# Optimization experiments

Measured on AMD Instinct MI355X. Metric: run time of the kernel, lower is better.

The kernel has to match this reference:

```python
import jax, jax.numpy as jnp
import numpy as np

N = 20000        # nodes
E = 160000       # edges
MUL = 64         # multiplicity per irrep (0e and 1o)
EDIM = 8         # scalar edge-embedding dim (radial basis)
NZ = 4           # node-attr (species one-hot) channels
AVG_NEIGH = 8.0  # avg_num_neighbors
INV_SQRT3 = float(1.0 / np.sqrt(3.0))  # CG norm for 1o x 1o -> 0e


def setup_inputs() -> dict:
    key = jax.random.key(0)
    ks = jax.random.split(key, 13)
    s = lambda fan: 1.0 / np.sqrt(fan)
    return {
        "node_feats": jax.random.normal(ks[0], (N, 256), jnp.float32),          # 64x0e | 64x1o (flattened)
        "node_attrs": jax.random.uniform(ks[1], (N, NZ), jnp.float32),
        "edge_attrs": jax.random.normal(ks[2], (E, 4), jnp.float32),            # SH lmax=1: [Y0 | Y1(3)]
        "edge_embedding": jax.random.normal(ks[3], (E, EDIM), jnp.float32),
        # linear_1 (per-irrep channel mixing)
        "W_lin1_0": jax.random.normal(ks[4], (MUL, MUL), jnp.float32),
        "W_lin1_1": jax.random.normal(ks[5], (MUL, MUL), jnp.float32),
        # radial MLP: EDIM -> EDIM -> 4*MUL tp weights
        "W_mlp1": jax.random.normal(ks[6], (EDIM, EDIM), jnp.float32),
        "W_mlp2": jax.random.normal(ks[7], (EDIM, 4 * MUL), jnp.float32),
        # linear_2: 128x0e+128x1o -> 128x0e+64x1o
        "W_lin2_0": jax.random.normal(ks[8], (2 * MUL, 2 * MUL), jnp.float32),
        "W_lin2_1": jax.random.normal(ks[9], (2 * MUL, MUL), jnp.float32),
        # self-connection FCTP weights: (u, z, w)
        "W_sc0": jax.random.normal(ks[10], (MUL, NZ, 2 * MUL), jnp.float32),
        "W_sc1": jax.random.normal(ks[11], (MUL, NZ, MUL), jnp.float32),
        "edge_index": jax.random.randint(ks[12], (2, E), 0, N, dtype=jnp.int32),
    }


def reference(node_feats, node_attrs, edge_attrs, edge_embedding,
              W_lin1_0, W_lin1_1, W_mlp1, W_mlp2,
              W_lin2_0, W_lin2_1, W_sc0, W_sc1, edge_index):
    edge_src, edge_dst = edge_index[0], edge_index[1]

    # split node feats into irrep blocks: 64x0e scalars, 64x1o vectors
    x0 = node_feats[:, :MUL]                         # [N, 64]
    x1 = node_feats[:, MUL:].reshape(N, MUL, 3)      # [N, 64, 3]

    # linear_1 (e3nn Linear, per-irrep, 1/sqrt(fan_in))
    inv = 1.0 / np.sqrt(MUL)
    h0 = (x0 @ W_lin1_0) * inv                       # [N, 64]
    h1 = jnp.einsum("nud,uv->nvd", x1, W_lin1_1) * inv

    # radial MLP -> per-edge UVU weights (e3nn FullyConnectedNet: no bias, silu, 1/sqrt(fan_in))
    inv_e = 1.0 / np.sqrt(EDIM)
    hid = jax.nn.silu((edge_embedding @ W_mlp1) * inv_e)
    w = (hid @ W_mlp2) * inv_e                       # [E, 4*MUL]
    w1, w2, w3, w4 = w[:, :MUL], w[:, MUL:2*MUL], w[:, 2*MUL:3*MUL], w[:, 3*MUL:]

    # gather source-node features per edge
    g0 = h0[edge_src]                                # [E, 64]
    g1 = h1[edge_src]                                # [E, 64, 3]
    a0 = edge_attrs[:, :1]                           # [E, 1]  Y0
    a1 = edge_attrs[:, 1:]                           # [E, 3]  Y1

    # UVU tensor product paths (v = 1 for SH attrs)
    m0_a = w1 * g0 * a0                              # 0e x 0e -> 0e
    m0_b = w4 * jnp.einsum("eud,ed->eu", g1, a1) * INV_SQRT3   # 1o x 1o -> 0e
    m1_a = (w2 * g0)[:, :, None] * a1[:, None, :]    # 0e x 1o -> 1o
    m1_b = (w3[:, :, None] * g1) * a0[:, :, None]    # 1o x 0e -> 1o
    msg0 = jnp.concatenate([m0_a, m0_b], axis=1)     # [E, 128]
    msg1 = jnp.concatenate([m1_a, m1_b], axis=1)     # [E, 128, 3]

    # scatter_add to destination nodes, normalize by sqrt(avg_num_neighbors)
    inv_n = 1.0 / np.sqrt(AVG_NEIGH)
    s0 = jax.ops.segment_sum(msg0, edge_dst, num_segments=N) * inv_n   # [N, 128]
    s1 = jax.ops.segment_sum(msg1, edge_dst, num_segments=N) * inv_n   # [N, 128, 3]

    # linear_2: 128x0e+128x1o -> 128x0e (64 scalars + 64 gates) + 64x1o
    inv2 = 1.0 / np.sqrt(2 * MUL)
    u0 = (s0 @ W_lin2_0) * inv2                      # [N, 128]
    u1 = jnp.einsum("nud,uw->nwd", s1, W_lin2_1) * inv2   # [N, 64, 3]

    # self-connection FCTP with 0e node attrs (species-conditioned linear)
    inv_sc = 1.0 / np.sqrt(MUL * NZ)
    sc0 = jnp.einsum("nu,nz,uzw->nw", x0, node_attrs, W_sc0) * inv_sc
    sc1 = jnp.einsum("nud,nz,uzw->nwd", x1, node_attrs, W_sc1) * inv_sc
    t0 = u0 + sc0                                    # [N, 128]
    t1 = u1 + sc1                                    # [N, 64, 3]

    # Gate nonlinearity: silu on scalars, silu(gates) * vectors
    scalars = jax.nn.silu(t0[:, :MUL])               # [N, 64]
    gates = jax.nn.silu(t0[:, MUL:])                 # [N, 64]
    vectors = gates[:, :, None] * t1                 # [N, 64, 3]

    out = jnp.concatenate([scalars, vectors.reshape(N, MUL * 3)], axis=1)  # [N, 256]
    # resnet (irreps match input)
    return node_feats + out
```

## Files before the change

kernel.cpp:

```cpp
#include <hip/hip_runtime.h>
#include <hip/hip_bf16.h>
#include <math.h>

#define N 20000
#define E 160000
#define MUL 64
#define EDIM 8
#define NZ 4

#define INV_SQRT_MUL 0.125f
#define INV_E 0.35355339059327373f
#define INV_N 0.35355339059327373f
#define INV2 0.08838834764831845f
#define INV_SC 0.0625f
#define INV_SQRT3 0.5773502691896258f

typedef unsigned short u16;
typedef unsigned int u32;
typedef short bf16x8 __attribute__((ext_vector_type(8)));
typedef float f32x4 __attribute__((ext_vector_type(4)));

__device__ __forceinline__ float silu(float v) {
    return v / (1.0f + __expf(-v));
}
__device__ __forceinline__ u16 f2bf(float f) {
    union { float f; unsigned int u; } v; v.f = f;
    unsigned int r = (v.u + 0x7FFFu + ((v.u >> 16) & 1u)) >> 16;
    return (u16)r;
}
__device__ __forceinline__ float bflo(u32 p) {
    union { unsigned int u; float f; } v; v.u = p << 16; return v.f;
}
__device__ __forceinline__ float bfhi(u32 p) {
    union { unsigned int u; float f; } v; v.u = p & 0xFFFF0000u; return v.f;
}
#define MFMA(a, b, c) __builtin_amdgcn_mfma_f32_16x16x32_bf16(a, b, c, 0, 0, 0)


#define PREP_B  5000
#define WCONV_B 320
#define HID_B   5000
#define LIST_B  625

__global__ __launch_bounds__(256) void k_front(
    const float* __restrict__ x, const float* __restrict__ attrs,
    const float* __restrict__ eemb, const int* __restrict__ eidx,
    const float* __restrict__ W20, const float* __restrict__ Wsc0,
    const float* __restrict__ W21, const float* __restrict__ Wsc1,
    const float* __restrict__ W0, const float* __restrict__ W1,
    const float* __restrict__ Wm1,
    u16* __restrict__ A1, u16* __restrict__ A2, u16* __restrict__ x1p,
    u16* __restrict__ Bt1m, u16* __restrict__ Bt1z, u16* __restrict__ Bt2,
    u16* __restrict__ W0b, u16* __restrict__ W1b,
    float* __restrict__ hid, int* __restrict__ head, int2* __restrict__ nl)
{
    const int b = blockIdx.x;
    const int tid = threadIdx.x;
    __shared__ float xr[4][256];

    if (b < PREP_B) {
        const int n0 = b * 4;
        #pragma unroll
        for (int t = 0; t < 4; ++t)
            xr[t][tid] = x[(size_t)(n0 + t) * 256 + tid];
        __syncthreads();
        #pragma unroll
        for (int t = 0; t < 4; ++t) {
            const int n = n0 + t;
            const float at = attrs[(size_t)n * 4 + (tid & 3)] * INV_SC;
            const int u = tid >> 2;
            #pragma unroll
            for (int d = 0; d < 3; ++d)
                A2[((size_t)n * 3 + d) * 384 + 128 + tid] = f2bf(xr[t][64 + u * 3 + d] * at);
            if (tid < 64) {
                A1[(size_t)n * 192 + 128 + tid] = f2bf(xr[t][tid]);
            } else {
                int q = tid - 64;
                int d = q >> 6, uu = q & 63;
                x1p[((size_t)n * 3 + d) * 64 + uu] = f2bf(xr[t][64 + uu * 3 + d]);
            }
        }
    } else if (b < PREP_B + WCONV_B) {
        int i = (b - PREP_B) * 256 + tid;
        if (i < 16384) {
            int w = i >> 7, k = i & 127;
            Bt1m[i] = f2bf(W20[k * 128 + w]);
        } else if (i < 49152) {
            int j = i - 16384;
            int z = j >> 13, r = j & 8191, w = r >> 6, k = r & 63;
            Bt1z[j] = f2bf(Wsc0[(k * 4 + z) * 128 + w] * INV_SC);
        } else if (i < 73728) {
            int j = i - 49152;
            int w = j / 384, k = j % 384;
            float v = (k < 128) ? W21[k * 64 + w] : Wsc1[(k - 128) * 64 + w];
            Bt2[j] = f2bf(v);
        } else if (i < 77824) {
            int j = i - 73728;
            int v = j >> 6, u = j & 63;
            W0b[j] = f2bf(W0[u * 64 + v] * INV_SQRT_MUL);
        } else {
            int j = i - 77824;
            int v = j >> 6, u = j & 63;
            W1b[j] = f2bf(W1[u * 64 + v] * INV_SQRT_MUL);
        }
    } else if (b < PREP_B + WCONV_B + HID_B) {
        int i = (b - PREP_B - WCONV_B) * 256 + tid;
        int e = i >> 3, k = i & 7;
        float s = 0.f;
        #pragma unroll
        for (int j = 0; j < 8; ++j)
            s += eemb[(size_t)e * 8 + j] * Wm1[j * 8 + k];
        hid[i] = silu(s * INV_E);
    } else {
        int e = (b - PREP_B - WCONV_B - HID_B) * 256 + tid;
        if (e < E) {
            int src = eidx[e];
            int dst = eidx[E + e];
            int old = atomicExch(&head[dst], e);
            nl[e] = make_int2(old, src);
        }
    }
}

__global__ __launch_bounds__(256) void k_hgemm(
    const u16* __restrict__ A1, const u16* __restrict__ x1p,
    const u16* __restrict__ W0b, const u16* __restrict__ W1b,
    u16* __restrict__ hc)
{
    const int lane = threadIdx.x & 63;
    const int g = blockIdx.x * 4 + (threadIdx.x >> 6);
    const int quad = lane >> 4, l16 = lane & 15;
    const bool isC1 = (g >= 1250);
    const int row0 = isC1 ? (g - 1250) * 16 : g * 16;
    const u16* Ap = isC1 ? (x1p + (size_t)(row0 + l16) * 64)
                         : (A1 + (size_t)(row0 + l16) * 192 + 128);
    const u16* Bp = isC1 ? W1b : W0b;

    f32x4 acc[4] = {};
    #pragma unroll
    for (int k0 = 0; k0 < 64; k0 += 32) {
        bf16x8 a = *(const bf16x8*)(Ap + k0 + quad * 8);
        #pragma unroll
        for (int ct = 0; ct < 4; ++ct) {
            bf16x8 bb = *(const bf16x8*)(Bp + (size_t)(ct * 16 + l16) * 64 + k0 + quad * 8);
            acc[ct] = MFMA(a, bb, acc[ct]);
        }
    }
    #pragma unroll
    for (int ct = 0; ct < 4; ++ct) {
        #pragma unroll
        for (int r = 0; r < 4; ++r) {
            int row = row0 + quad * 4 + r;
            int vv = ct * 16 + l16;
            if (!isC1) {
                hc[(size_t)row * 256 + vv * 4] = f2bf(acc[ct][r]);
            } else {
                int n = row / 3, d = row - 3 * (row / 3);
                hc[(size_t)n * 256 + vv * 4 + 1 + d] = f2bf(acc[ct][r]);
            }
        }
    }
}

__global__ __launch_bounds__(256) void k_gather(
    const int* __restrict__ head, const int2* __restrict__ nl,
    const float* __restrict__ eattr, const float* __restrict__ hid,
    const u32* __restrict__ hc2, const float* __restrict__ Wm2,
    u16* __restrict__ A1, u16* __restrict__ A2)
{
    const int lane = threadIdx.x & 63;
    const int n = blockIdx.x * 4 + (threadIdx.x >> 6);

    float wm0[8], wm1[8], wm2r[8], wm3[8];
    #pragma unroll
    for (int k = 0; k < 8; ++k) {
        wm0[k]  = Wm2[k * 256 + lane];
        wm1[k]  = Wm2[k * 256 + 64 + lane];
        wm2r[k] = Wm2[k * 256 + 128 + lane];
        wm3[k]  = Wm2[k * 256 + 192 + lane];
    }

    float acc0a = 0.f, acc0b = 0.f;
    float s1a[3] = {0.f, 0.f, 0.f}, s1b[3] = {0.f, 0.f, 0.f};

    int e = head[n];
    if (e != -1) {
        int2 v = nl[e];
        while (true) {
            const int en = v.x;
            int2 vn;
            if (en != -1) vn = nl[en];

            const float4 ea = ((const float4*)eattr)[e];
            const float4 hA = ((const float4*)hid)[(size_t)e * 2];
            const float4 hB = ((const float4*)hid)[(size_t)e * 2 + 1];
            const uint2  hp = ((const uint2*)hc2)[(size_t)v.y * 64 + lane];

            float w1 = hA.x*wm0[0]+hA.y*wm0[1]+hA.z*wm0[2]+hA.w*wm0[3]
                     + hB.x*wm0[4]+hB.y*wm0[5]+hB.z*wm0[6]+hB.w*wm0[7];
            float w2 = hA.x*wm1[0]+hA.y*wm1[1]+hA.z*wm1[2]+hA.w*wm1[3]
                     + hB.x*wm1[4]+hB.y*wm1[5]+hB.z*wm1[6]+hB.w*wm1[7];
            float w3 = hA.x*wm2r[0]+hA.y*wm2r[1]+hA.z*wm2r[2]+hA.w*wm2r[3]
                     + hB.x*wm2r[4]+hB.y*wm2r[5]+hB.z*wm2r[6]+hB.w*wm2r[7];
            float w4 = hA.x*wm3[0]+hA.y*wm3[1]+hA.z*wm3[2]+hA.w*wm3[3]
                     + hB.x*wm3[4]+hB.y*wm3[5]+hB.z*wm3[6]+hB.w*wm3[7];
            const float g0 = bflo(hp.x), g1x = bfhi(hp.x);
            const float g1y = bflo(hp.y), g1z = bfhi(hp.y);
            acc0a += w1 * g0 * ea.x;
            acc0b += w4 * (g1x * ea.y + g1y * ea.z + g1z * ea.w);
            const float wg = w2 * g0, w3a = w3 * ea.x;
            s1a[0] += wg * ea.y;  s1a[1] += wg * ea.z;  s1a[2] += wg * ea.w;
            s1b[0] += w3a * g1x;  s1b[1] += w3a * g1y;  s1b[2] += w3a * g1z;

            if (en == -1) break;
            e = en; v = vn;
        }
    }

    const float f = INV_E * INV_N * INV2;
    u16* a1p = &A1[(size_t)n * 192];
    a1p[lane]      = f2bf(acc0a * f);
    a1p[64 + lane] = f2bf(acc0b * f * INV_SQRT3);
    #pragma unroll
    for (int d = 0; d < 3; ++d) {
        u16* a2p = &A2[((size_t)n * 3 + d) * 384];
        a2p[lane]      = f2bf(s1a[d] * f);
        a2p[64 + lane] = f2bf(s1b[d] * f);
    }
}

__global__ __launch_bounds__(256) void k_gemm_fused(
    const u16* __restrict__ A1, const u16* __restrict__ A2,
    const u16* __restrict__ Bt1m, const u16* __restrict__ Bt1z,
    const u16* __restrict__ Bt2,
    const float* __restrict__ attrs, const float* __restrict__ x,
    float* __restrict__ out)
{
    const int lane = threadIdx.x & 63;
    const int wave = threadIdx.x >> 6;
    const int quad = lane >> 4, l16 = lane & 15;
    const int n0 = blockIdx.x * 16;

    __shared__ float st0[16][132];
    __shared__ float st1[48][68];
    __shared__ float sat[16][4];
    if (threadIdx.x < 64)
        sat[threadIdx.x >> 2][threadIdx.x & 3] =
            attrs[(size_t)(n0 + (threadIdx.x >> 2)) * 4 + (threadIdx.x & 3)];

    const u16* a0p  = A1 + (size_t)(n0 + l16) * 192 + quad * 8;
    const u16* a1p  = A2 + (size_t)(3 * n0 + l16) * 384 + quad * 8;
    const u16* b0p  = Bt1m + (size_t)(wave * 16 + l16) * 128 + quad * 8;
    const u16* b1p  = Bt1m + (size_t)((wave + 4) * 16 + l16) * 128 + quad * 8;
    const u16* bz0p = Bt1z + (size_t)(wave * 16 + l16) * 64 + quad * 8;
    const u16* bz1p = Bt1z + (size_t)((wave + 4) * 16 + l16) * 64 + quad * 8;
    const u16* b2p  = Bt2 + (size_t)(wave * 16 + l16) * 384 + quad * 8;

    f32x4 m0 = {}, m1 = {}, m2 = {}, m3 = {}, m4 = {};
    f32x4 z0[4] = {}, z1[4] = {};

    #pragma unroll
    for (int kt = 0; kt < 12; ++kt) {
        const int ko = kt * 32;
        bf16x8 a1 = *(const bf16x8*)(a1p + ko);
        bf16x8 a2 = *(const bf16x8*)(a1p + 16 * 384 + ko);
        bf16x8 a3 = *(const bf16x8*)(a1p + 32 * 384 + ko);
        bf16x8 b2 = *(const bf16x8*)(b2p + ko);
        m2 = MFMA(a1, b2, m2);
        m3 = MFMA(a2, b2, m3);
        m4 = MFMA(a3, b2, m4);
    }
    #pragma unroll
    for (int kt = 0; kt < 4; ++kt) {
        const int ko = kt * 32;
        bf16x8 a0 = *(const bf16x8*)(a0p + ko);
        bf16x8 b0 = *(const bf16x8*)(b0p + ko);
        bf16x8 b1 = *(const bf16x8*)(b1p + ko);
        m0 = MFMA(a0, b0, m0);
        m1 = MFMA(a0, b1, m1);
    }
    #pragma unroll
    for (int kt = 0; kt < 2; ++kt) {
        const int ko = kt * 32;
        bf16x8 a0 = *(const bf16x8*)(a0p + 128 + ko);
        #pragma unroll
        for (int z = 0; z < 4; ++z) {
            bf16x8 c0 = *(const bf16x8*)(bz0p + z * 8192 + ko);
            bf16x8 c1 = *(const bf16x8*)(bz1p + z * 8192 + ko);
            z0[z] = MFMA(a0, c0, z0[z]);
            z1[z] = MFMA(a0, c1, z1[z]);
        }
    }
    __syncthreads();

    #pragma unroll
    for (int r = 0; r < 4; ++r) {
        const int r0 = quad * 4 + r;
        const float ta = sat[r0][0], tb = sat[r0][1],
                    tc = sat[r0][2], td = sat[r0][3];
        st0[r0][wave * 16 + l16] =
            m0[r] + ta * z0[0][r] + tb * z0[1][r] + tc * z0[2][r] + td * z0[3][r];
        st0[r0][(wave + 4) * 16 + l16] =
            m1[r] + ta * z1[0][r] + tb * z1[1][r] + tc * z1[2][r] + td * z1[3][r];
        st1[r0][wave * 16 + l16]      = m2[r];
        st1[16 + r0][wave * 16 + l16] = m3[r];
        st1[32 + r0][wave * 16 + l16] = m4[r];
    }
    __syncthreads();

    const int c = threadIdx.x;
    #pragma unroll
    for (int t = 0; t < 16; ++t) {
        const float xv = x[(size_t)(n0 + t) * 256 + c];
        float o;
        if (c < 64) {
            o = xv + silu(st0[t][c]);
        } else {
            int r = c - 64;
            int w = (r * 21846) >> 16;
            int d = r - w * 3;
            o = xv + silu(st0[t][64 + w]) * st1[t * 3 + d][w];
        }
        out[(size_t)(n0 + t) * 256 + c] = o;
    }
}

extern "C" void kernel_launch(void* const* d_in, const int* in_sizes, int n_in,
                              void* d_out, int out_size, void* d_ws, size_t ws_size,
                              hipStream_t stream) {
    const float* node_feats = (const float*)d_in[0];
    const float* node_attrs = (const float*)d_in[1];
    const float* edge_attrs = (const float*)d_in[2];
    const float* edge_emb   = (const float*)d_in[3];
    const float* W_lin1_0   = (const float*)d_in[4];
    const float* W_lin1_1   = (const float*)d_in[5];
    const float* W_mlp1     = (const float*)d_in[6];
    const float* W_mlp2     = (const float*)d_in[7];
    const float* W_lin2_0   = (const float*)d_in[8];
    const float* W_lin2_1   = (const float*)d_in[9];
    const float* W_sc0      = (const float*)d_in[10];
    const float* W_sc1      = (const float*)d_in[11];
    const int*   edge_index = (const int*)d_in[12];
    float* out = (float*)d_out;

    char* p = (char*)d_ws;
    float* hid = (float*)p;                 p += (size_t)E * 8 * 4;
    u16* hc    = (u16*)p;                   p += (size_t)N * 256 * 2;
    u16* A1    = (u16*)p;                   p += (size_t)N * 192 * 2;
    u16* A2    = (u16*)p;                   p += (size_t)N * 3 * 384 * 2;
    u16* x1p   = (u16*)p;                   p += (size_t)N * 3 * 64 * 2;
    u16* Bt1m  = (u16*)p;                   p += 16384 * 2;
    u16* Bt1z  = (u16*)p;                   p += 32768 * 2;
    u16* Bt2   = (u16*)p;                   p += 24576 * 2;
    u16* W0b   = (u16*)p;                   p += 4096 * 2;
    u16* W1b   = (u16*)p;                   p += 4096 * 2;
    int* head  = (int*)p;                   p += N * 4;
    int2* nl   = (int2*)p;                  p += (size_t)E * 8;

    hipMemsetAsync(head, 0xFF, N * sizeof(int), stream);

    k_front<<<PREP_B + WCONV_B + HID_B + LIST_B, 256, 0, stream>>>(
        node_feats, node_attrs, edge_emb, edge_index,
        W_lin2_0, W_sc0, W_lin2_1, W_sc1, W_lin1_0, W_lin1_1, W_mlp1,
        A1, A2, x1p, Bt1m, Bt1z, Bt2, W0b, W1b, hid, head, nl);
    k_hgemm<<<1250, 256, 0, stream>>>(A1, x1p, W0b, W1b, hc);
    k_gather<<<N / 4, 256, 0, stream>>>(head, nl, edge_attrs, hid,
                                        (const u32*)hc, W_mlp2, A1, A2);
    k_gemm_fused<<<1250, 256, 0, stream>>>(A1, A2, Bt1m, Bt1z, Bt2,
                                           node_attrs, node_feats, out);
}
```

Before: 222.1 us.

## Build attr-scaled vector operand in-register in GEMM and software-pipeline gather loads

The front kernel no longer writes the 256-wide attr-scaled x1 block into A2. The fused GEMM now forms that operand on the fly from x1p and node attributes when building MFMA fragments, and A2 shrinks to 128 columns. The gather loop also prefetches the next edge's attributes, hidden values and hc row one iteration ahead to hide pointer-chasing latency. This removes a large intermediate write and read, at the cost of extra VALU conversion work inside the GEMM inner loop and more registers in the gather.

```diff
diff --git a/kernel.cpp b/kernel.cpp
--- a/kernel.cpp
+++ b/kernel.cpp
@@ -43,13 +43,13 @@
 #define LIST_B  625
 
 __global__ __launch_bounds__(256) void k_front(
-    const float* __restrict__ x, const float* __restrict__ attrs,
+    const float* __restrict__ x,
     const float* __restrict__ eemb, const int* __restrict__ eidx,
     const float* __restrict__ W20, const float* __restrict__ Wsc0,
     const float* __restrict__ W21, const float* __restrict__ Wsc1,
     const float* __restrict__ W0, const float* __restrict__ W1,
     const float* __restrict__ Wm1,
-    u16* __restrict__ A1, u16* __restrict__ A2, u16* __restrict__ x1p,
+    u16* __restrict__ A1, u16* __restrict__ x1p,
     u16* __restrict__ Bt1m, u16* __restrict__ Bt1z, u16* __restrict__ Bt2,
     u16* __restrict__ W0b, u16* __restrict__ W1b,
     float* __restrict__ hid, int* __restrict__ head, int2* __restrict__ nl)
@@ -67,11 +67,6 @@
         #pragma unroll
         for (int t = 0; t < 4; ++t) {
             const int n = n0 + t;
-            const float at = attrs[(size_t)n * 4 + (tid & 3)] * INV_SC;
-            const int u = tid >> 2;
-            #pragma unroll
-            for (int d = 0; d < 3; ++d)
-                A2[((size_t)n * 3 + d) * 384 + 128 + tid] = f2bf(xr[t][64 + u * 3 + d] * at);
             if (tid < 64) {
                 A1[(size_t)n * 192 + 128 + tid] = f2bf(xr[t][tid]);
             } else {
@@ -166,7 +161,7 @@
     const int* __restrict__ head, const int2* __restrict__ nl,
     const float* __restrict__ eattr, const float* __restrict__ hid,
     const u32* __restrict__ hc2, const float* __restrict__ Wm2,
-    u16* __restrict__ A1, u16* __restrict__ A2)
+    u16* __restrict__ A1, u16* __restrict__ A2g)
 {
     const int lane = threadIdx.x & 63;
     const int n = blockIdx.x * 4 + (threadIdx.x >> 6);
@@ -183,18 +178,29 @@
     float acc0a = 0.f, acc0b = 0.f;
     float s1a[3] = {0.f, 0.f, 0.f}, s1b[3] = {0.f, 0.f, 0.f};
 
-    int e = head[n];
-    if (e != -1) {
-        int2 v = nl[e];
+    int e0 = head[n];
+    if (e0 != -1) {
+        int2 v0 = nl[e0];
+        float4 ea = ((const float4*)eattr)[e0];
+        float4 hA = ((const float4*)hid)[(size_t)e0 * 2];
+        float4 hB = ((const float4*)hid)[(size_t)e0 * 2 + 1];
+        uint2  hp = ((const uint2*)hc2)[(size_t)v0.y * 64 + lane];
+        int e1 = v0.x;
+        int2 v1 = make_int2(-1, 0);
+        if (e1 != -1) v1 = nl[e1];
+
         while (true) {
-            const int en = v.x;
-            int2 vn;
-            if (en != -1) vn = nl[en];
-
-            const float4 ea = ((const float4*)eattr)[e];
-            const float4 hA = ((const float4*)hid)[(size_t)e * 2];
-            const float4 hB = ((const float4*)hid)[(size_t)e * 2 + 1];
-            const uint2  hp = ((const uint2*)hc2)[(size_t)v.y * 64 + lane];
+            int e2 = -1;
+            int2 v2 = make_int2(-1, 0);
+            float4 eaN, hAN, hBN; uint2 hpN;
+            if (e1 != -1) {
+                e2 = v1.x;
+                if (e2 != -1) v2 = nl[e2];
+                eaN = ((const float4*)eattr)[e1];
+                hAN = ((const float4*)hid)[(size_t)e1 * 2];
+                hBN = ((const float4*)hid)[(size_t)e1 * 2 + 1];
+                hpN = ((const uint2*)hc2)[(size_t)v1.y * 64 + lane];
+            }
 
             float w1 = hA.x*wm0[0]+hA.y*wm0[1]+hA.z*wm0[2]+hA.w*wm0[3]
                      + hB.x*wm0[4]+hB.y*wm0[5]+hB.z*wm0[6]+hB.w*wm0[7];
@@ -212,8 +218,9 @@
             s1a[0] += wg * ea.y;  s1a[1] += wg * ea.z;  s1a[2] += wg * ea.w;
             s1b[0] += w3a * g1x;  s1b[1] += w3a * g1y;  s1b[2] += w3a * g1z;
 
-            if (en == -1) break;
-            e = en; v = vn;
+            if (e1 == -1) break;
+            ea = eaN; hA = hAN; hB = hBN; hp = hpN;
+            e1 = e2; v1 = v2;
         }
     }
 
@@ -223,14 +230,15 @@
     a1p[64 + lane] = f2bf(acc0b * f * INV_SQRT3);
     #pragma unroll
     for (int d = 0; d < 3; ++d) {
-        u16* a2p = &A2[((size_t)n * 3 + d) * 384];
+        u16* a2p = &A2g[((size_t)n * 3 + d) * 128];
         a2p[lane]      = f2bf(s1a[d] * f);
         a2p[64 + lane] = f2bf(s1b[d] * f);
     }
 }
 
 __global__ __launch_bounds__(256) void k_gemm_fused(
-    const u16* __restrict__ A1, const u16* __restrict__ A2,
+    const u16* __restrict__ A1, const u16* __restrict__ A2g,
+    const u16* __restrict__ x1p,
     const u16* __restrict__ Bt1m, const u16* __restrict__ Bt1z,
     const u16* __restrict__ Bt2,
     const float* __restrict__ attrs, const float* __restrict__ x,
@@ -247,28 +255,60 @@
     if (threadIdx.x < 64)
         sat[threadIdx.x >> 2][threadIdx.x & 3] =
             attrs[(size_t)(n0 + (threadIdx.x >> 2)) * 4 + (threadIdx.x & 3)];
-
-    const u16* a0p  = A1 + (size_t)(n0 + l16) * 192 + quad * 8;
-    const u16* a1p  = A2 + (size_t)(3 * n0 + l16) * 384 + quad * 8;
+    __syncthreads();
+
+    float atv[3][4];
+    #pragma unroll
+    for (int rt = 0; rt < 3; ++rt) {
+        const int ro = rt * 16 + l16;
+        const int nn = (ro * 21846) >> 16;
+        #pragma unroll
+        for (int z = 0; z < 4; ++z) atv[rt][z] = sat[nn][z] * INV_SC;
+    }
+
+    const u16* a0p  = A1  + (size_t)(n0 + l16) * 192 + quad * 8;
+    const u16* a1p  = A2g + (size_t)(3 * n0 + l16) * 128 + quad * 8;
     const u16* b0p  = Bt1m + (size_t)(wave * 16 + l16) * 128 + quad * 8;
     const u16* b1p  = Bt1m + (size_t)((wave + 4) * 16 + l16) * 128 + quad * 8;
     const u16* bz0p = Bt1z + (size_t)(wave * 16 + l16) * 64 + quad * 8;
     const u16* bz1p = Bt1z + (size_t)((wave + 4) * 16 + l16) * 64 + quad * 8;
     const u16* b2p  = Bt2 + (size_t)(wave * 16 + l16) * 384 + quad * 8;
-
-    f32x4 m0 = {}, m1 = {}, m2 = {}, m3 = {}, m4 = {};
+    const u16* xq0  = x1p + (size_t)(3 * n0 + l16) * 64 + quad * 2;
+    const u16* xq1  = x1p + (size_t)(3 * n0 + 16 + l16) * 64 + quad * 2;
+    const u16* xq2  = x1p + (size_t)(3 * n0 + 32 + l16) * 64 + quad * 2;
+
+    f32x4 m0 = {}, m1 = {};
+    f32x4 mt[3] = {};
     f32x4 z0[4] = {}, z1[4] = {};
 
     #pragma unroll
-    for (int kt = 0; kt < 12; ++kt) {
+    for (int kt = 0; kt < 4; ++kt) {
         const int ko = kt * 32;
         bf16x8 a1 = *(const bf16x8*)(a1p + ko);
-        bf16x8 a2 = *(const bf16x8*)(a1p + 16 * 384 + ko);
-        bf16x8 a3 = *(const bf16x8*)(a1p + 32 * 384 + ko);
+        bf16x8 a2 = *(const bf16x8*)(a1p + 16 * 128 + ko);
+        bf16x8 a3 = *(const bf16x8*)(a1p + 32 * 128 + ko);
         bf16x8 b2 = *(const bf16x8*)(b2p + ko);
-        m2 = MFMA(a1, b2, m2);
-        m3 = MFMA(a2, b2, m3);
-        m4 = MFMA(a3, b2, m4);
+        mt[0] = MFMA(a1, b2, mt[0]);
+        mt[1] = MFMA(a2, b2, mt[1]);
+        mt[2] = MFMA(a3, b2, mt[2]);
+    }
+    #pragma unroll
+    for (int kt = 0; kt < 8; ++kt) {
+        bf16x8 b2 = *(const bf16x8*)(b2p + 128 + kt * 32);
+        const u32 xpa = *(const u32*)(xq0 + kt * 8);
+        const u32 xpb = *(const u32*)(xq1 + kt * 8);
+        const u32 xpc = *(const u32*)(xq2 + kt * 8);
+        #pragma unroll
+        for (int rt = 0; rt < 3; ++rt) {
+            const u32 xp = (rt == 0) ? xpa : (rt == 1) ? xpb : xpc;
+            const float xa = bflo(xp), xb = bfhi(xp);
+            bf16x8 af;
+            #pragma unroll
+            for (int j = 0; j < 4; ++j) af[j] = (short)f2bf(xa * atv[rt][j]);
+            #pragma unroll
+            for (int j = 0; j < 4; ++j) af[4 + j] = (short)f2bf(xb * atv[rt][j]);
+            mt[rt] = MFMA(af, b2, mt[rt]);
+        }
     }
     #pragma unroll
     for (int kt = 0; kt < 4; ++kt) {
@@ -302,9 +342,9 @@
             m0[r] + ta * z0[0][r] + tb * z0[1][r] + tc * z0[2][r] + td * z0[3][r];
         st0[r0][(wave + 4) * 16 + l16] =
             m1[r] + ta * z1[0][r] + tb * z1[1][r] + tc * z1[2][r] + td * z1[3][r];
-        st1[r0][wave * 16 + l16]      = m2[r];
-        st1[16 + r0][wave * 16 + l16] = m3[r];
-        st1[32 + r0][wave * 16 + l16] = m4[r];
+        st1[r0][wave * 16 + l16]      = mt[0][r];
+        st1[16 + r0][wave * 16 + l16] = mt[1][r];
+        st1[32 + r0][wave * 16 + l16] = mt[2][r];
     }
     __syncthreads();
 
@@ -347,7 +387,7 @@
     float* hid = (float*)p;                 p += (size_t)E * 8 * 4;
     u16* hc    = (u16*)p;                   p += (size_t)N * 256 * 2;
     u16* A1    = (u16*)p;                   p += (size_t)N * 192 * 2;
-    u16* A2    = (u16*)p;                   p += (size_t)N * 3 * 384 * 2;
+    u16* A2g   = (u16*)p;                   p += (size_t)N * 3 * 128 * 2;
     u16* x1p   = (u16*)p;                   p += (size_t)N * 3 * 64 * 2;
     u16* Bt1m  = (u16*)p;                   p += 16384 * 2;
     u16* Bt1z  = (u16*)p;                   p += 32768 * 2;
@@ -360,12 +400,12 @@
     hipMemsetAsync(head, 0xFF, N * sizeof(int), stream);
 
     k_front<<<PREP_B + WCONV_B + HID_B + LIST_B, 256, 0, stream>>>(
-        node_feats, node_attrs, edge_emb, edge_index,
+        node_feats, edge_emb, edge_index,
         W_lin2_0, W_sc0, W_lin2_1, W_sc1, W_lin1_0, W_lin1_1, W_mlp1,
-        A1, A2, x1p, Bt1m, Bt1z, Bt2, W0b, W1b, hid, head, nl);
+        A1, x1p, Bt1m, Bt1z, Bt2, W0b, W1b, hid, head, nl);
     k_hgemm<<<1250, 256, 0, stream>>>(A1, x1p, W0b, W1b, hc);
     k_gather<<<N / 4, 256, 0, stream>>>(head, nl, edge_attrs, hid,
-                                        (const u32*)hc, W_mlp2, A1, A2);
-    k_gemm_fused<<<1250, 256, 0, stream>>>(A1, A2, Bt1m, Bt1z, Bt2,
+                                        (const u32*)hc, W_mlp2, A1, A2g);
+    k_gemm_fused<<<1250, 256, 0, stream>>>(A1, A2g, x1p, Bt1m, Bt1z, Bt2,
                                            node_attrs, node_feats, out);
 }
```

Result: faster. 213.3 us (-4.0%).
